# Performance work log

Hardware: AMD Instinct MI355X
Metric: run time of the kernel (lower is better)

The kernel has to match this reference:

```python
import jax, jax.numpy as jnp
import numpy as np

N = 50000      # nodes
E = 800000     # edges
D = 256        # hidden_dim (input node features)
A = 128        # attention_dim = attention_ratio * heads
H = 8          # heads
DK = A // H    # 16


def setup_inputs() -> dict:
    key = jax.random.key(0)
    ks = jax.random.split(key, 6)
    x = jax.random.normal(ks[0], (N, D), dtype=jnp.float32)
    # small weight scale keeps exp(pre) well-conditioned (module uses tiny const init)
    Wq = jax.random.normal(ks[1], (A, D), dtype=jnp.float32) * 0.02
    bq = jnp.full((A,), 0.01, dtype=jnp.float32)
    Wk = jax.random.normal(ks[2], (A, D), dtype=jnp.float32) * 0.02
    bk = jnp.full((A,), 0.01, dtype=jnp.float32)
    edge_index = jax.random.randint(ks[3], (2, E), 0, N, dtype=jnp.int32)
    # d0_index[1] holds the two node indices each duplicated edge score scatters to
    d0_index = jax.random.randint(ks[4], (2, 2 * E), 0, N, dtype=jnp.int32)
    return {"x": x, "Wq": Wq, "bq": bq, "Wk": Wk, "bk": bk,
            "edge_index": edge_index, "d0_index": d0_index}


def reference(x, Wq, bq, Wk, bk, edge_index, d0_index):
    # linear projections -> [N, H, DK]
    q = (x @ Wq.T + bq).reshape(N, H, DK)
    k = (x @ Wk.T + bk).reshape(N, H, DK)
    src, dst = edge_index[0], edge_index[1]
    q_i = q[src]   # [E, H, DK]
    k_j = k[dst]
    q_j = q[dst]
    k_i = k[src]
    # symmetrized scaled-dot attention score per edge/head
    pre = 0.5 * jnp.sum(q_i * k_j + q_j * k_i, axis=-1)  # [E, H]
    pre = jnp.mean(pre, axis=-1)                          # [E]
    diagA1 = jnp.exp(pre)
    # duplicate each edge score: (a, a, b, b, ...) == torch (view(-1,1)*ones(E,2)).view(-1)
    edge_score_per_node = jnp.repeat(diagA1, 2)           # [2E]
    diagA0 = jax.ops.segment_sum(edge_score_per_node, d0_index[1], num_segments=N)
    return diagA0, diagA1
```

## Files before the change

### kernel.cpp

```cpp
#include <hip/hip_runtime.h>
#include <hip/hip_bf16.h>

#define N_NODES 50000
#define N_EDGES 800000
#define DIM 256
#define QKDIM 256
#define NB_T  391
#define NBLK_P 391
#define SLOT  32
#define CAPB  (NBLK_P * SLOT)
#define ITEMS (2 * N_EDGES)
#define IPB   4096
#define EDGE_BLOCKS (N_EDGES / 64)

typedef __bf16 bfrag  __attribute__((ext_vector_type(8)));
typedef __bf16 bf4    __attribute__((ext_vector_type(4)));
typedef float  ffrag  __attribute__((ext_vector_type(4)));
typedef float  f2     __attribute__((ext_vector_type(2)));
typedef float  f4v    __attribute__((ext_vector_type(4)));

#define EP_PITCH 272

__global__ __launch_bounds__(256) void proj_fly(
    const float* __restrict__ x,
    const float* __restrict__ Wq, const float* __restrict__ Wk,
    const float* __restrict__ bq, const float* __restrict__ bk,
    unsigned char* __restrict__ qk8)
{
    __shared__ __bf16 As[64 * 256];

    const int tid  = threadIdx.x;
    const int wv   = tid >> 6;
    const int lane = tid & 63;
    const int m    = lane & 15;
    const int q    = lane >> 4;
    const int mbase = blockIdx.x * 64;

    {
        const int srow = tid >> 2;
        const int c4   = tid & 3;
        int grow = mbase + srow;
        grow = grow < N_NODES ? grow : N_NODES - 1;
        const float* xp = x + (size_t)grow * DIM;
        const int mt_ = srow >> 4, m_ = srow & 15;
        #pragma unroll
        for (int i = 0; i < 16; ++i) {
            const int k = c4 * 4 + 16 * i;
            const f4v v = __builtin_nontemporal_load((const f4v*)(xp + k));
            bf4 o;
            o[0] = (__bf16)v[0]; o[1] = (__bf16)v[1];
            o[2] = (__bf16)v[2]; o[3] = (__bf16)v[3];
            const int seg = (k >> 5) * 4 + mt_;
            const int ln  = ((k >> 3) & 3) * 16 + m_;
            *(bf4*)(As + seg * 512 + ln * 8 + (k & 7)) = o;
        }
    }
    __syncthreads();

    ffrag acc[4][4] = {};

    #pragma unroll
    for (int h = 0; h < 2; ++h) {
        bfrag b[4][4];
        #pragma unroll
        for (int sp = 0; sp < 4; ++sp)
            #pragma unroll
            for (int nt = 0; nt < 4; ++nt) {
                const int col = wv * 64 + nt * 16 + m;
                const float* wrow = (col < 128)
                    ? (Wq + (size_t)col * DIM)
                    : (Wk + (size_t)(col - 128) * DIM);
                const int k0 = 32 * (4 * h + sp) + 8 * q;
                const float4 f0 = *(const float4*)(wrow + k0);
                const float4 f1 = *(const float4*)(wrow + k0 + 4);
                bfrag o;
                o[0] = (__bf16)f0.x; o[1] = (__bf16)f0.y;
                o[2] = (__bf16)f0.z; o[3] = (__bf16)f0.w;
                o[4] = (__bf16)f1.x; o[5] = (__bf16)f1.y;
                o[6] = (__bf16)f1.z; o[7] = (__bf16)f1.w;
                b[sp][nt] = o;
            }
        #pragma unroll
        for (int sp = 0; sp < 4; ++sp) {
            bfrag a[4];
            #pragma unroll
            for (int mt = 0; mt < 4; ++mt)
                a[mt] = *(const bfrag*)(As + ((4 * h + sp) * 4 + mt) * 512 + lane * 8);
            #pragma unroll
            for (int mt = 0; mt < 4; ++mt)
                #pragma unroll
                for (int nt = 0; nt < 4; ++nt)
                    acc[mt][nt] = __builtin_amdgcn_mfma_f32_16x16x32_bf16(
                                      a[mt], b[sp][nt], acc[mt][nt], 0, 0, 0);
        }
    }

    __syncthreads();
    unsigned char* ep = (unsigned char*)As;
    #pragma unroll
    for (int nt = 0; nt < 4; ++nt) {
        const int col  = wv * 64 + nt * 16 + m;
        const float bias = (col < 128) ? bq[col] : bk[col - 128];
        #pragma unroll
        for (int mt = 0; mt < 4; ++mt) {
            #pragma unroll
            for (int r = 0; r < 4; ++r) {
                const int rl = mt * 16 + q * 4 + r;
                const float v = acc[mt][nt][r] + bias;
                const int pk = __builtin_amdgcn_cvt_pk_fp8_f32(v, v, 0, false);
                ep[rl * EP_PITCH + col] = (unsigned char)(pk & 0xFF);
            }
        }
    }
    __syncthreads();
    {
        const int rl = tid >> 2;
        const int ch = tid & 3;
        const int grow = mbase + rl;
        if (grow < N_NODES) {
            const uint4* s4 = (const uint4*)(ep + rl * EP_PITCH + ch * 64);
            const uint4 t0 = s4[0], t1 = s4[1], t2 = s4[2], t3 = s4[3];
            uint4* g = (uint4*)(qk8 + (size_t)grow * QKDIM + ch * 64);
            g[0] = t0; g[1] = t1; g[2] = t2; g[3] = t3;
        }
    }
}

__global__ __launch_bounds__(256) void edge_bin(
    const unsigned char* __restrict__ qk8,
    const int* __restrict__ edge_index,
    float* __restrict__ out,
    const int* __restrict__ d0, unsigned int* __restrict__ rec,
    unsigned char* __restrict__ cnts)
{
    __shared__ int lcnt[NB_T];
    const int tid = threadIdx.x;

    if (blockIdx.x >= NBLK_P) {
        const int eb = blockIdx.x - NBLK_P;
        const int wave = (eb << 2) + (tid >> 6);
        const int lane = tid & 63;
        const int g = lane >> 2;
        const int j = lane & 3;
        const int e = wave * 16 + g;

        const int src = __builtin_nontemporal_load(edge_index + e);
        const int dst = __builtin_nontemporal_load(edge_index + N_EDGES + e);

        const uint4* rs = (const uint4*)(qk8 + (size_t)src * QKDIM);
        const uint4* rd = (const uint4*)(qk8 + (size_t)dst * QKDIM);

        uint4 a[4], b[4];
        #pragma unroll
        for (int i = 0; i < 4; ++i) a[i] = rs[4 * i + j];
        #pragma unroll
        for (int i = 0; i < 4; ++i) b[i] = rd[4 * ((i + 2) & 3) + j];

        f2 acc = {0.f, 0.f};
        #pragma unroll
        for (int i = 0; i < 4; ++i) {
            const unsigned int* ua = (const unsigned int*)&a[i];
            const unsigned int* ub = (const unsigned int*)&b[i];
            #pragma unroll
            for (int t = 0; t < 4; ++t) {
                const f2 x0 = __builtin_amdgcn_cvt_pk_f32_fp8(ua[t], false);
                const f2 y0 = __builtin_amdgcn_cvt_pk_f32_fp8(ub[t], false);
                const f2 x1 = __builtin_amdgcn_cvt_pk_f32_fp8(ua[t], true);
                const f2 y1 = __builtin_amdgcn_cvt_pk_f32_fp8(ub[t], true);
                acc += x0 * y0;
                acc += x1 * y1;
            }
        }
        float p = acc[0] + acc[1];
        p += __shfl_xor(p, 1, 64);
        p += __shfl_xor(p, 2, 64);

        if (j == 0)
            out[N_NODES + e] = __expf(p * 0.0625f);
        return;
    }

    const int pb = blockIdx.x;

    for (int b = tid; b < NB_T; b += 256) lcnt[b] = 0;
    __syncthreads();
    const int base = pb * IPB;
    int tg[16];
    #pragma unroll
    for (int r = 0; r < 16; ++r) {
        const int i = base + r * 256 + tid;
        tg[r] = (i < ITEMS) ? d0[i] : -1;
        if (tg[r] >= 0) atomicAdd(&lcnt[tg[r] >> 7], 1);
    }
    __syncthreads();
    for (int b = tid; b < NB_T; b += 256) {
        const int c = lcnt[b];
        cnts[(size_t)pb * NB_T + b] = (unsigned char)(c < SLOT ? c : SLOT);
        lcnt[b] = 0;
    }
    __syncthreads();
    #pragma unroll
    for (int r = 0; r < 16; ++r) {
        if (tg[r] >= 0) {
            const int i = base + r * 256 + tid;
            const int b = tg[r] >> 7;
            const int off = atomicAdd(&lcnt[b], 1);
            if (off < SLOT)
                rec[(size_t)b * CAPB + pb * SLOT + off] =
                    ((unsigned int)(tg[r] & 127) << 20) | (unsigned int)(i >> 1);
        }
    }
}

__global__ __launch_bounds__(1024) void phase_scatter(
    const unsigned int* __restrict__ rec, const unsigned char* __restrict__ cnts,
    float* __restrict__ out)
{
    __shared__ float acc[16][128];
    __shared__ unsigned char lc[NBLK_P];
    const int b = blockIdx.x;
    const int tid = threadIdx.x;
    const int wid = tid >> 6;
    for (int i = tid; i < 16 * 128; i += 1024) ((float*)acc)[i] = 0.f;
    if (tid < NBLK_P) lc[tid] = cnts[(size_t)tid * NB_T + b];
    __syncthreads();

    const unsigned int* rb = rec + (size_t)b * CAPB;
    for (int s = tid; s < CAPB; s += 1024) {
        const int blk = s >> 5;
        const int off = s & (SLOT - 1);
        if (off < (int)lc[blk]) {
            const unsigned int r = rb[s];
            const float v = out[N_NODES + (r & 0xFFFFF)];
            atomicAdd(&acc[wid][r >> 20], v);
        }
    }
    __syncthreads();

    if (tid < 128) {
        float s = 0.f;
        #pragma unroll
        for (int w = 0; w < 16; ++w) s += acc[w][tid];
        const int n = b * 128 + tid;
        if (n < N_NODES) out[n] = s;
    }
}

__global__ __launch_bounds__(256) void edge_atomic(
    const unsigned char* __restrict__ qk8,
    const int* __restrict__ edge_index, const int* __restrict__ d0,
    float* __restrict__ out)
{
    const int wave = (blockIdx.x * blockDim.x + threadIdx.x) >> 6;
    const int lane = threadIdx.x & 63;
    const int g = lane >> 2, j = lane & 3;
    const int e = wave * 16 + g;

    const int src = edge_index[e];
    const int dst = edge_index[N_EDGES + e];

    const uint4* rs = (const uint4*)(qk8 + (size_t)src * QKDIM);
    const uint4* rd = (const uint4*)(qk8 + (size_t)dst * QKDIM);

    uint4 a[4], b[4];
    #pragma unroll
    for (int i = 0; i < 4; ++i) a[i] = rs[4 * i + j];
    #pragma unroll
    for (int i = 0; i < 4; ++i) b[i] = rd[4 * ((i + 2) & 3) + j];

    f2 acc = {0.f, 0.f};
    #pragma unroll
    for (int i = 0; i < 4; ++i) {
        const unsigned int* ua = (const unsigned int*)&a[i];
        const unsigned int* ub = (const unsigned int*)&b[i];
        #pragma unroll
        for (int t = 0; t < 4; ++t) {
            const f2 x0 = __builtin_amdgcn_cvt_pk_f32_fp8(ua[t], false);
            const f2 y0 = __builtin_amdgcn_cvt_pk_f32_fp8(ub[t], false);
            const f2 x1 = __builtin_amdgcn_cvt_pk_f32_fp8(ua[t], true);
            const f2 y1 = __builtin_amdgcn_cvt_pk_f32_fp8(ub[t], true);
            acc += x0 * y0;
            acc += x1 * y1;
        }
    }
    float p = acc[0] + acc[1];
    p += __shfl_xor(p, 1, 64);
    p += __shfl_xor(p, 2, 64);

    if (j < 2) {
        const float val = __expf(p * 0.0625f);
        if (j == 0) out[N_NODES + e] = val;
        atomicAdd(&out[d0[2 * e + j]], val);
    }
}


extern "C" void kernel_launch(void* const* d_in, const int* in_sizes, int n_in,
                              void* d_out, int out_size, void* d_ws, size_t ws_size,
                              hipStream_t stream) {
    const float* x  = (const float*)d_in[0];
    const float* Wq = (const float*)d_in[1];
    const float* bq = (const float*)d_in[2];
    const float* Wk = (const float*)d_in[3];
    const float* bk = (const float*)d_in[4];
    const int* edge_index = (const int*)d_in[5];
    const int* d0 = (const int*)d_in[6] + 2 * N_EDGES;
    float* out = (float*)d_out;

    char* w = (char*)d_ws;
    unsigned char* qk8 = (unsigned char*)w;  w += (size_t)N_NODES * QKDIM;
    unsigned int* rec = (unsigned int*)w;    w += (size_t)NB_T * CAPB * 4;
    unsigned char* cnts = (unsigned char*)w; w += (size_t)NBLK_P * NB_T;

    const size_t need = (size_t)(w - (char*)d_ws);
    const int use_bin = (ws_size >= need) ? 1 : 0;

    if (use_bin) {
        proj_fly<<<(N_NODES + 63) / 64, 256, 0, stream>>>(x, Wq, Wk, bq, bk, qk8);
        edge_bin<<<NBLK_P + EDGE_BLOCKS, 256, 0, stream>>>(
            qk8, edge_index, out, d0, rec, cnts);
        phase_scatter<<<NB_T, 1024, 0, stream>>>(rec, cnts, out);
    } else {
        hipMemsetAsync(out, 0, N_NODES * sizeof(float), stream);
        proj_fly<<<(N_NODES + 63) / 64, 256, 0, stream>>>(x, Wq, Wk, bq, bk, qk8);
        edge_atomic<<<N_EDGES / 64, 256, 0, stream>>>(qk8, edge_index, d0, out);
    }
}
```

Baseline: 205.7 us.

## Fuse d0 binning into the projection kernel and split edge scoring out

Moves the d0 binning work so it runs alongside the projection GEMM in one launch, using shared memory that the two block roles reuse. Edge scoring becomes its own kernel launched after the projection, so there are still three launches. The aim is to overlap the memory-bound binning with the compute-bound projection instead of with edge scoring. The cost is that edge scoring no longer overlaps with binning, and the fallback path now also does the binning work it does not need.

Result: no change. 201.9 us (-1.8%).

```diff
diff --git a/kernel.cpp b/kernel.cpp
--- a/kernel.cpp
+++ b/kernel.cpp
@@ -11,7 +11,7 @@
 #define CAPB  (NBLK_P * SLOT)
 #define ITEMS (2 * N_EDGES)
 #define IPB   4096
-#define EDGE_BLOCKS (N_EDGES / 64)
+#define PROJ_BLOCKS 782
 
 typedef __bf16 bfrag  __attribute__((ext_vector_type(8)));
 typedef __bf16 bf4    __attribute__((ext_vector_type(4)));
@@ -21,165 +21,117 @@
 
 #define EP_PITCH 272
 
-__global__ __launch_bounds__(256) void proj_fly(
+__global__ __launch_bounds__(256) void proj_bin(
     const float* __restrict__ x,
     const float* __restrict__ Wq, const float* __restrict__ Wk,
     const float* __restrict__ bq, const float* __restrict__ bk,
-    unsigned char* __restrict__ qk8)
-{
-    __shared__ __bf16 As[64 * 256];
-
-    const int tid  = threadIdx.x;
-    const int wv   = tid >> 6;
-    const int lane = tid & 63;
-    const int m    = lane & 15;
-    const int q    = lane >> 4;
-    const int mbase = blockIdx.x * 64;
-
-    {
-        const int srow = tid >> 2;
-        const int c4   = tid & 3;
-        int grow = mbase + srow;
-        grow = grow < N_NODES ? grow : N_NODES - 1;
-        const float* xp = x + (size_t)grow * DIM;
-        const int mt_ = srow >> 4, m_ = srow & 15;
-        #pragma unroll
-        for (int i = 0; i < 16; ++i) {
-            const int k = c4 * 4 + 16 * i;
-            const f4v v = __builtin_nontemporal_load((const f4v*)(xp + k));
-            bf4 o;
-            o[0] = (__bf16)v[0]; o[1] = (__bf16)v[1];
-            o[2] = (__bf16)v[2]; o[3] = (__bf16)v[3];
-            const int seg = (k >> 5) * 4 + mt_;
-            const int ln  = ((k >> 3) & 3) * 16 + m_;
-            *(bf4*)(As + seg * 512 + ln * 8 + (k & 7)) = o;
-        }
-    }
-    __syncthreads();
-
-    ffrag acc[4][4] = {};
-
-    #pragma unroll
-    for (int h = 0; h < 2; ++h) {
-        bfrag b[4][4];
-        #pragma unroll
-        for (int sp = 0; sp < 4; ++sp)
-            #pragma unroll
-            for (int nt = 0; nt < 4; ++nt) {
-                const int col = wv * 64 + nt * 16 + m;
-                const float* wrow = (col < 128)
-                    ? (Wq + (size_t)col * DIM)
-                    : (Wk + (size_t)(col - 128) * DIM);
-                const int k0 = 32 * (4 * h + sp) + 8 * q;
-                const float4 f0 = *(const float4*)(wrow + k0);
-                const float4 f1 = *(const float4*)(wrow + k0 + 4);
-                bfrag o;
-                o[0] = (__bf16)f0.x; o[1] = (__bf16)f0.y;
-                o[2] = (__bf16)f0.z; o[3] = (__bf16)f0.w;
-                o[4] = (__bf16)f1.x; o[5] = (__bf16)f1.y;
-                o[6] = (__bf16)f1.z; o[7] = (__bf16)f1.w;
-                b[sp][nt] = o;
-            }
-        #pragma unroll
-        for (int sp = 0; sp < 4; ++sp) {
-            bfrag a[4];
-            #pragma unroll
-            for (int mt = 0; mt < 4; ++mt)
-                a[mt] = *(const bfrag*)(As + ((4 * h + sp) * 4 + mt) * 512 + lane * 8);
-            #pragma unroll
-            for (int mt = 0; mt < 4; ++mt)
-                #pragma unroll
-                for (int nt = 0; nt < 4; ++nt)
-                    acc[mt][nt] = __builtin_amdgcn_mfma_f32_16x16x32_bf16(
-                                      a[mt], b[sp][nt], acc[mt][nt], 0, 0, 0);
-        }
-    }
-
-    __syncthreads();
-    unsigned char* ep = (unsigned char*)As;
-    #pragma unroll
-    for (int nt = 0; nt < 4; ++nt) {
-        const int col  = wv * 64 + nt * 16 + m;
-        const float bias = (col < 128) ? bq[col] : bk[col - 128];
-        #pragma unroll
-        for (int mt = 0; mt < 4; ++mt) {
-            #pragma unroll
-            for (int r = 0; r < 4; ++r) {
-                const int rl = mt * 16 + q * 4 + r;
-                const float v = acc[mt][nt][r] + bias;
-                const int pk = __builtin_amdgcn_cvt_pk_fp8_f32(v, v, 0, false);
-                ep[rl * EP_PITCH + col] = (unsigned char)(pk & 0xFF);
-            }
-        }
-    }
-    __syncthreads();
-    {
-        const int rl = tid >> 2;
-        const int ch = tid & 3;
-        const int grow = mbase + rl;
-        if (grow < N_NODES) {
-            const uint4* s4 = (const uint4*)(ep + rl * EP_PITCH + ch * 64);
-            const uint4 t0 = s4[0], t1 = s4[1], t2 = s4[2], t3 = s4[3];
-            uint4* g = (uint4*)(qk8 + (size_t)grow * QKDIM + ch * 64);
-            g[0] = t0; g[1] = t1; g[2] = t2; g[3] = t3;
-        }
-    }
-}
-
-__global__ __launch_bounds__(256) void edge_bin(
-    const unsigned char* __restrict__ qk8,
-    const int* __restrict__ edge_index,
-    float* __restrict__ out,
+    unsigned char* __restrict__ qk8,
     const int* __restrict__ d0, unsigned int* __restrict__ rec,
     unsigned char* __restrict__ cnts)
 {
-    __shared__ int lcnt[NB_T];
+    __shared__ unsigned char smem[32768];
     const int tid = threadIdx.x;
 
     if (blockIdx.x >= NBLK_P) {
-        const int eb = blockIdx.x - NBLK_P;
-        const int wave = (eb << 2) + (tid >> 6);
+        __bf16* As = (__bf16*)smem;
+        const int wv   = tid >> 6;
         const int lane = tid & 63;
-        const int g = lane >> 2;
-        const int j = lane & 3;
-        const int e = wave * 16 + g;
-
-        const int src = __builtin_nontemporal_load(edge_index + e);
-        const int dst = __builtin_nontemporal_load(edge_index + N_EDGES + e);
-
-        const uint4* rs = (const uint4*)(qk8 + (size_t)src * QKDIM);
-        const uint4* rd = (const uint4*)(qk8 + (size_t)dst * QKDIM);
-
-        uint4 a[4], b[4];
-        #pragma unroll
-        for (int i = 0; i < 4; ++i) a[i] = rs[4 * i + j];
-        #pragma unroll
-        for (int i = 0; i < 4; ++i) b[i] = rd[4 * ((i + 2) & 3) + j];
-
-        f2 acc = {0.f, 0.f};
-        #pragma unroll
-        for (int i = 0; i < 4; ++i) {
-            const unsigned int* ua = (const unsigned int*)&a[i];
-            const unsigned int* ub = (const unsigned int*)&b[i];
+        const int m    = lane & 15;
+        const int q    = lane >> 4;
+        const int mbase = (blockIdx.x - NBLK_P) * 64;
+
+        {
+            const int srow = tid >> 2;
+            const int c4   = tid & 3;
+            int grow = mbase + srow;
+            grow = grow < N_NODES ? grow : N_NODES - 1;
+            const float* xp = x + (size_t)grow * DIM;
+            const int mt_ = srow >> 4, m_ = srow & 15;
             #pragma unroll
-            for (int t = 0; t < 4; ++t) {
-                const f2 x0 = __builtin_amdgcn_cvt_pk_f32_fp8(ua[t], false);
-                const f2 y0 = __builtin_amdgcn_cvt_pk_f32_fp8(ub[t], false);
-                const f2 x1 = __builtin_amdgcn_cvt_pk_f32_fp8(ua[t], true);
-                const f2 y1 = __builtin_amdgcn_cvt_pk_f32_fp8(ub[t], true);
-                acc += x0 * y0;
-                acc += x1 * y1;
+            for (int i = 0; i < 16; ++i) {
+                const int k = c4 * 4 + 16 * i;
+                const f4v v = __builtin_nontemporal_load((const f4v*)(xp + k));
+                bf4 o;
+                o[0] = (__bf16)v[0]; o[1] = (__bf16)v[1];
+                o[2] = (__bf16)v[2]; o[3] = (__bf16)v[3];
+                const int seg = (k >> 5) * 4 + mt_;
+                const int ln  = ((k >> 3) & 3) * 16 + m_;
+                *(bf4*)(As + seg * 512 + ln * 8 + (k & 7)) = o;
             }
         }
-        float p = acc[0] + acc[1];
-        p += __shfl_xor(p, 1, 64);
-        p += __shfl_xor(p, 2, 64);
-
-        if (j == 0)
-            out[N_NODES + e] = __expf(p * 0.0625f);
+        __syncthreads();
+
+        ffrag acc[4][4] = {};
+
+        #pragma unroll
+        for (int h = 0; h < 2; ++h) {
+            bfrag b[4][4];
+            #pragma unroll
+            for (int sp = 0; sp < 4; ++sp)
+                #pragma unroll
+                for (int nt = 0; nt < 4; ++nt) {
+                    const int col = wv * 64 + nt * 16 + m;
+                    const float* wrow = (col < 128)
+                        ? (Wq + (size_t)col * DIM)
+                        : (Wk + (size_t)(col - 128) * DIM);
+                    const int k0 = 32 * (4 * h + sp) + 8 * q;
+                    const float4 f0 = *(const float4*)(wrow + k0);
+                    const float4 f1 = *(const float4*)(wrow + k0 + 4);
+                    bfrag o;
+                    o[0] = (__bf16)f0.x; o[1] = (__bf16)f0.y;
+                    o[2] = (__bf16)f0.z; o[3] = (__bf16)f0.w;
+                    o[4] = (__bf16)f1.x; o[5] = (__bf16)f1.y;
+                    o[6] = (__bf16)f1.z; o[7] = (__bf16)f1.w;
+                    b[sp][nt] = o;
+                }
+            #pragma unroll
+            for (int sp = 0; sp < 4; ++sp) {
+                bfrag a[4];
+                #pragma unroll
+                for (int mt = 0; mt < 4; ++mt)
+                    a[mt] = *(const bfrag*)(As + ((4 * h + sp) * 4 + mt) * 512 + lane * 8);
+                #pragma unroll
+                for (int mt = 0; mt < 4; ++mt)
+                    #pragma unroll
+                    for (int nt = 0; nt < 4; ++nt)
+                        acc[mt][nt] = __builtin_amdgcn_mfma_f32_16x16x32_bf16(
+                                          a[mt], b[sp][nt], acc[mt][nt], 0, 0, 0);
+            }
+        }
+
+        __syncthreads();
+        unsigned char* ep = (unsigned char*)As;
+        #pragma unroll
+        for (int nt = 0; nt < 4; ++nt) {
+            const int col  = wv * 64 + nt * 16 + m;
+            const float bias = (col < 128) ? bq[col] : bk[col - 128];
+            #pragma unroll
+            for (int mt = 0; mt < 4; ++mt) {
+                #pragma unroll
+                for (int r = 0; r < 4; ++r) {
+                    const int rl = mt * 16 + q * 4 + r;
+                    const float v = acc[mt][nt][r] + bias;
+                    const int pk = __builtin_amdgcn_cvt_pk_fp8_f32(v, v, 0, false);
+                    ep[rl * EP_PITCH + col] = (unsigned char)(pk & 0xFF);
+                }
+            }
+        }
+        __syncthreads();
+        {
+            const int rl = tid >> 2;
+            const int ch = tid & 3;
+            const int grow = mbase + rl;
+            if (grow < N_NODES) {
+                const uint4* s4 = (const uint4*)(ep + rl * EP_PITCH + ch * 64);
+                const uint4 t0 = s4[0], t1 = s4[1], t2 = s4[2], t3 = s4[3];
+                uint4* g = (uint4*)(qk8 + (size_t)grow * QKDIM + ch * 64);
+                g[0] = t0; g[1] = t1; g[2] = t2; g[3] = t3;
+            }
+        }
         return;
     }
 
+    int* lcnt = (int*)smem;
     const int pb = blockIdx.x;
 
     for (int b = tid; b < NB_T; b += 256) lcnt[b] = 0;
@@ -210,6 +162,52 @@
                     ((unsigned int)(tg[r] & 127) << 20) | (unsigned int)(i >> 1);
         }
     }
+}
+
+__global__ __launch_bounds__(256) void edge_compute(
+    const unsigned char* __restrict__ qk8,
+    const int* __restrict__ edge_index,
+    float* __restrict__ out)
+{
+    const int wave = (blockIdx.x * blockDim.x + threadIdx.x) >> 6;
+    const int lane = threadIdx.x & 63;
+    const int g = lane >> 2;
+    const int j = lane & 3;
+    const int e = wave * 16 + g;
+
+    const int src = __builtin_nontemporal_load(edge_index + e);
+    const int dst = __builtin_nontemporal_load(edge_index + N_EDGES + e);
+
+    const uint4* rs = (const uint4*)(qk8 + (size_t)src * QKDIM);
+    const uint4* rd = (const uint4*)(qk8 + (size_t)dst * QKDIM);
+
+    uint4 a[4], b[4];
+    #pragma unroll
+    for (int i = 0; i < 4; ++i) a[i] = rs[4 * i + j];
+    #pragma unroll
+    for (int i = 0; i < 4; ++i) b[i] = rd[4 * ((i + 2) & 3) + j];
+
+    f2 acc = {0.f, 0.f};
+    #pragma unroll
+    for (int i = 0; i < 4; ++i) {
+        const unsigned int* ua = (const unsigned int*)&a[i];
+        const unsigned int* ub = (const unsigned int*)&b[i];
+        #pragma unroll
+        for (int t = 0; t < 4; ++t) {
+            const f2 x0 = __builtin_amdgcn_cvt_pk_f32_fp8(ua[t], false);
+            const f2 y0 = __builtin_amdgcn_cvt_pk_f32_fp8(ub[t], false);
+            const f2 x1 = __builtin_amdgcn_cvt_pk_f32_fp8(ua[t], true);
+            const f2 y1 = __builtin_amdgcn_cvt_pk_f32_fp8(ub[t], true);
+            acc += x0 * y0;
+            acc += x1 * y1;
+        }
+    }
+    float p = acc[0] + acc[1];
+    p += __shfl_xor(p, 1, 64);
+    p += __shfl_xor(p, 2, 64);
+
+    if (j == 0)
+        out[N_NODES + e] = __expf(p * 0.0625f);
 }
 
 __global__ __launch_bounds__(1024) void phase_scatter(
@@ -316,13 +314,14 @@
     const int use_bin = (ws_size >= need) ? 1 : 0;
 
     if (use_bin) {
-        proj_fly<<<(N_NODES + 63) / 64, 256, 0, stream>>>(x, Wq, Wk, bq, bk, qk8);
-        edge_bin<<<NBLK_P + EDGE_BLOCKS, 256, 0, stream>>>(
-            qk8, edge_index, out, d0, rec, cnts);
+        proj_bin<<<NBLK_P + PROJ_BLOCKS, 256, 0, stream>>>(
+            x, Wq, Wk, bq, bk, qk8, d0, rec, cnts);
+        edge_compute<<<N_EDGES / 64, 256, 0, stream>>>(qk8, edge_index, out);
         phase_scatter<<<NB_T, 1024, 0, stream>>>(rec, cnts, out);
     } else {
         hipMemsetAsync(out, 0, N_NODES * sizeof(float), stream);
-        proj_fly<<<(N_NODES + 63) / 64, 256, 0, stream>>>(x, Wq, Wk, bq, bk, qk8);
+        proj_bin<<<NBLK_P + PROJ_BLOCKS, 256, 0, stream>>>(
+            x, Wq, Wk, bq, bk, qk8, d0, rec, cnts);
         edge_atomic<<<N_EDGES / 64, 256, 0, stream>>>(qk8, edge_index, d0, out);
     }
 }
```
